# Optimization experiments

Hardware: AMD Instinct MI355X
Metric: run time of the kernel (lower is better)

The kernel has to match this reference:

```python
import jax, jax.numpy as jnp
import numpy as np

NUM_HEADS = 16
LN_EPS = 1e-12


def setup_inputs() -> dict:
    key = jax.random.key(0)
    ks = jax.random.split(key, 4)
    L, B, D = 2048, 2, 1024
    x = jax.random.normal(ks[0], (L, B, D), dtype=jnp.float32)
    attention_mask = jax.random.randint(ks[1], (B, L), 0, 2, dtype=jnp.int32)
    ln_w = jnp.ones((D,), dtype=jnp.float32)
    ln_b = jnp.zeros((D,), dtype=jnp.float32)
    qkv_w = jax.random.normal(ks[2], (3 * D, D), dtype=jnp.float32) * 0.02
    qkv_b = jnp.zeros((3 * D,), dtype=jnp.float32)
    out_w = jax.random.normal(ks[3], (D, D), dtype=jnp.float32) * 0.02
    out_b = jnp.zeros((D,), dtype=jnp.float32)
    return {"x": x, "attention_mask": attention_mask, "ln_w": ln_w, "ln_b": ln_b,
            "qkv_w": qkv_w, "qkv_b": qkv_b, "out_w": out_w, "out_b": out_b}


def _layer_norm(x, w, b):
    mu = jnp.mean(x, axis=-1, keepdims=True)
    var = jnp.mean(jnp.square(x - mu), axis=-1, keepdims=True)
    return (x - mu) * jax.lax.rsqrt(var + LN_EPS) * w + b


def reference(x, attention_mask, ln_w, ln_b, qkv_w, qkv_b, out_w, out_b):
    L, B, D = x.shape
    H = NUM_HEADS
    hd = D // H
    scale = 1.0 / np.sqrt(hd).astype(np.float32)

    xn = _layer_norm(x, ln_w, ln_b)                       # (L, B, D)
    qkv = xn @ qkv_w.T + qkv_b                            # (L, B, 3D)
    q, k, v = jnp.split(qkv, 3, axis=-1)
    # (L, B, D) -> (L, B*H, hd) -> (B*H, L, hd)
    q = q.reshape(L, B * H, hd).swapaxes(0, 1)
    k = k.reshape(L, B * H, hd).swapaxes(0, 1)
    v = v.reshape(L, B * H, hd).swapaxes(0, 1)

    scores = jnp.einsum('nld,nmd->nlm', q, k) * scale     # (B*H, L, L)
    mask = jnp.broadcast_to(attention_mask[:, None, :], (B, H, L)).reshape(B * H, 1, L)
    scores = jnp.where(mask == 0, -jnp.inf, scores)
    probs = jax.nn.softmax(scores, axis=-1)               # masked cols -> 0
    # dropout prob = 0.0 -> identity
    context = jnp.einsum('nlm,nmd->nld', probs, v)        # (B*H, L, hd)
    context = context.swapaxes(0, 1).reshape(L, B, D)
    return context @ out_w.T + out_b
```

## Files before the change

kernel.cpp:

```cpp
#include <hip/hip_runtime.h>
#include <hip/hip_bf16.h>
#include <cstdint>

static constexpr int LSEQ = 2048;
static constexpr int BB   = 2;
static constexpr int DM   = 1024;
static constexpr int NHD  = 16;
static constexpr int HD   = 64;
static constexpr int ROWS = LSEQ * BB;
static constexpr int NQKV = 3 * DM;

typedef __attribute__((ext_vector_type(8)))  short v8s;
typedef __attribute__((ext_vector_type(4)))  float v4f;
typedef __attribute__((ext_vector_type(16))) float v16f;
typedef __attribute__((ext_vector_type(4)))  unsigned int v4u;

#if __has_builtin(__builtin_amdgcn_exp2f)
#define EXP2F(x) __builtin_amdgcn_exp2f(x)
#else
#define EXP2F(x) __expf((x) * 0.69314718056f)
#endif

static constexpr float QSCALE = 0.125f * 1.44269504089f;
static constexpr float NEGM   = -10.0f * 1.44269504089f;

__device__ __forceinline__ unsigned short f2bf(float f) {
    unsigned int u = __builtin_bit_cast(unsigned int, f);
    u += 0x7fffu + ((u >> 16) & 1u);
    return (unsigned short)(u >> 16);
}

__device__ __forceinline__ void gload_lds16(const void* g, void* l) {
    auto gp = (const __attribute__((address_space(1))) unsigned int*)(uintptr_t)g;
    auto lp = (__attribute__((address_space(3))) unsigned int*)(uintptr_t)l;
    __builtin_amdgcn_global_load_lds(gp, lp, 16, 0, 0);
}

__global__ __launch_bounds__(256) void cast_w_kernel(const float* __restrict__ qkv_w,
                                                     const float* __restrict__ out_w,
                                                     unsigned short* __restrict__ wq,
                                                     unsigned short* __restrict__ wo) {
    size_t i = ((size_t)blockIdx.x * 256 + threadIdx.x) * 8;
    const float* src; unsigned short* dst; size_t off;
    if (i < (size_t)NQKV * DM) { src = qkv_w; dst = wq; off = i; }
    else                       { src = out_w; dst = wo; off = i - (size_t)NQKV * DM; }
    float4 a = *(const float4*)(src + off);
    float4 b = *(const float4*)(src + off + 4);
    ushort4 o0, o1;
    o0.x = f2bf(a.x); o0.y = f2bf(a.y); o0.z = f2bf(a.z); o0.w = f2bf(a.w);
    o1.x = f2bf(b.x); o1.y = f2bf(b.y); o1.z = f2bf(b.z); o1.w = f2bf(b.w);
    *(ushort4*)(dst + off)     = o0;
    *(ushort4*)(dst + off + 4) = o1;
}

__global__ __launch_bounds__(256) void ln_cast_kernel(const float* __restrict__ x,
                                                      const float* __restrict__ w,
                                                      const float* __restrict__ bia,
                                                      unsigned short* __restrict__ xn) {
    const int row = blockIdx.x;
    const int t = threadIdx.x;
    const float* xr = x + (size_t)row * DM;
    float4 v = ((const float4*)xr)[t];
    float s  = v.x + v.y + v.z + v.w;
    float sq = v.x*v.x + v.y*v.y + v.z*v.z + v.w*v.w;
    #pragma unroll
    for (int off = 32; off > 0; off >>= 1) {
        s  += __shfl_down(s, off);
        sq += __shfl_down(sq, off);
    }
    __shared__ float red[8];
    const int wv = t >> 6;
    if ((t & 63) == 0) { red[wv] = s; red[4 + wv] = sq; }
    __syncthreads();
    if (t == 0) {
        float S = red[0] + red[1] + red[2] + red[3];
        float Q = red[4] + red[5] + red[6] + red[7];
        float mu  = S * (1.0f / DM);
        float var = Q * (1.0f / DM) - mu * mu;
        red[0] = mu;
        red[1] = rsqrtf(var + 1e-12f);
    }
    __syncthreads();
    const float mu = red[0], rs = red[1];
    float4 wv4 = ((const float4*)w)[t];
    float4 bv4 = ((const float4*)bia)[t];
    ushort4 o;
    o.x = f2bf((v.x - mu) * rs * wv4.x + bv4.x);
    o.y = f2bf((v.y - mu) * rs * wv4.y + bv4.y);
    o.z = f2bf((v.z - mu) * rs * wv4.z + bv4.z);
    o.w = f2bf((v.w - mu) * rs * wv4.w + bv4.w);
    ((ushort4*)(xn + (size_t)row * DM))[t] = o;
}

template <int BM, int BN, int EPI>
__global__ __launch_bounds__(BM == 256 ? 512 : 256)
void gemm2_kernel(const unsigned short* __restrict__ A,
                  const unsigned short* __restrict__ Bt,
                  const float* __restrict__ bias,
                  float* __restrict__ outF,
                  unsigned short* __restrict__ qb,
                  unsigned short* __restrict__ kb,
                  unsigned short* __restrict__ vt,
                  int N) {
    constexpr int K  = DM;
    constexpr int NW = (BM == 256) ? 8 : 4;
    constexpr int NWN = NW / 2;
    constexpr int WM = BM / 2;
    constexpr int WN = BN / NWN;
    constexpr int MR = WM / 16;
    constexpr int FC = WN / 16;
    constexpr int NT = K / 64;
    __shared__ unsigned short Al[2][BM * 64];
    __shared__ unsigned short Bl[2][BN * 64];
    const int nbn = N / BN;
    const int bm = blockIdx.x / nbn;
    const int bn = blockIdx.x % nbn;
    const int tid = threadIdx.x;
    const int w = tid >> 6, lane = tid & 63;
    const int l15 = lane & 15, l4 = lane >> 4;
    const int wm = w / NWN, wn = w % NWN;
    const unsigned short* Ab = A  + (size_t)bm * BM * K;
    const unsigned short* Bb = Bt + (size_t)bn * BN * K;
    const int srow8  = lane >> 3;
    const int schunk = ((lane & 7) ^ (srow8 & 7)) * 8;
    const int swz    = l15 & 7;

    v4f acc[MR][FC] = {};

    auto STAGE = [&](int buf, int t) {
        const int k0 = t * 64;
        #pragma unroll
        for (int i = 0; i < BM / 8 / NW; ++i) {
            const int r0 = w * (BM / NW) + i * 8;
            gload_lds16(Ab + (size_t)(r0 + srow8) * K + k0 + schunk, &Al[buf][r0 * 64]);
        }
        #pragma unroll
        for (int i = 0; i < BN / 8 / NW; ++i) {
            const int r0 = w * (BN / NW) + i * 8;
            gload_lds16(Bb + (size_t)(r0 + srow8) * K + k0 + schunk, &Bl[buf][r0 * 64]);
        }
    };
    auto COMPUTE = [&](int buf) {
        #pragma unroll
        for (int ks = 0; ks < 2; ++ks) {
            v8s af[MR]; v8s bf[FC];
            #pragma unroll
            for (int m = 0; m < MR; ++m) {
                const int row = wm * WM + m * 16 + l15;
                af[m] = *(const v8s*)&Al[buf][row * 64 + ((ks * 4 + l4) ^ swz) * 8];
            }
            #pragma unroll
            for (int n = 0; n < FC; ++n) {
                const int row = wn * WN + n * 16 + l15;
                bf[n] = *(const v8s*)&Bl[buf][row * 64 + ((ks * 4 + l4) ^ swz) * 8];
            }
            #pragma unroll
            for (int m = 0; m < MR; ++m)
                #pragma unroll
                for (int n = 0; n < FC; ++n)
                    acc[m][n] = __builtin_amdgcn_mfma_f32_16x16x32_bf16(af[m], bf[n], acc[m][n], 0, 0, 0);
        }
    };

    STAGE(0, 0);
    __syncthreads();
    int cur = 0;
    for (int t = 0; t < NT - 1; ++t) {
        STAGE(cur ^ 1, t + 1);
        COMPUTE(cur);
        __syncthreads();
        cur ^= 1;
    }
    COMPUTE(cur);

    #pragma unroll
    for (int m = 0; m < MR; ++m) {
        #pragma unroll
        for (int n = 0; n < FC; ++n) {
            #pragma unroll
            for (int r = 0; r < 4; ++r) {
                const int row = bm * BM + wm * WM + m * 16 + l4 * 4 + r;
                const int col = bn * BN + wn * WN + n * 16 + l15;
                const float val = acc[m][n][r] + bias[col];
                if (EPI == 0) {
                    outF[(size_t)row * N + col] = val;
                } else {
                    const int lq = row >> 1, b = row & 1;
                    const int which = col >> 10, jr = col & 1023;
                    const int h = jr >> 6, d = jr & 63;
                    const int bh = b * NHD + h;
                    if (which == 0)      qb[((size_t)bh * LSEQ + lq) * HD + d] = f2bf(val * QSCALE);
                    else if (which == 1) kb[((size_t)bh * LSEQ + lq) * HD + d] = f2bf(val);
                    else                 vt[((size_t)bh * HD + d) * LSEQ + lq] = f2bf(val);
                }
            }
        }
    }
}

__global__ __launch_bounds__(256) void attn_kernel(const unsigned short* __restrict__ qbuf,
                                                   const unsigned short* __restrict__ kbuf,
                                                   const unsigned short* __restrict__ vtbuf,
                                                   const int* __restrict__ amask,
                                                   unsigned short* __restrict__ ctx) {
    __shared__ unsigned short Kl[2][64 * 64];
    __shared__ unsigned short Vl[2][64 * 64];
    __shared__ alignas(16) float mb_all[LSEQ];
    __shared__ alignas(16) float inv_l[4 * 32];
    const int id = blockIdx.x;
    const int inner = id >> 3;
    const int bh = (id & 7) * 4 + (inner & 3);
    const int qblk = inner >> 2;
    const int bat = bh >> 4, h = bh & 15;
    const int tid = threadIdx.x;
    const int w = tid >> 6, lane = tid & 63;
    const int l31 = lane & 31, hi = lane >> 5;
    const int q0 = qblk * 128 + w * 32;

    #pragma unroll
    for (int i = 0; i < LSEQ / 256; ++i)
        mb_all[i * 256 + tid] = amask[bat * LSEQ + i * 256 + tid] ? NEGM : -1e30f;

    const unsigned short* Qp = qbuf + ((size_t)bh * LSEQ + q0 + l31) * HD + hi * 8;
    v8s qfr[4];
    #pragma unroll
    for (int s = 0; s < 4; ++s) qfr[s] = *(const v8s*)(Qp + s * 16);

    const unsigned short* Kb = kbuf  + (size_t)bh * LSEQ * HD;
    const unsigned short* Vb = vtbuf + (size_t)bh * HD * LSEQ;

    v16f O0 = {}, O1 = {};
    float lsum = 0.f;

    const int srow = lane >> 3;
    const int schunk = ((lane & 7) ^ srow) * 8;
    const int rsw = l31 & 7;

    auto STAGE = [&](int buf, int kv0) {
        const int r0 = w * 16;
        gload_lds16(Kb + (size_t)(kv0 + r0 + srow) * HD + schunk,       &Kl[buf][r0 * 64]);
        gload_lds16(Kb + (size_t)(kv0 + r0 + 8 + srow) * HD + schunk,   &Kl[buf][(r0 + 8) * 64]);
        gload_lds16(Vb + (size_t)(r0 + srow) * LSEQ + kv0 + schunk,     &Vl[buf][r0 * 64]);
        gload_lds16(Vb + (size_t)(r0 + 8 + srow) * LSEQ + kv0 + schunk, &Vl[buf][(r0 + 8) * 64]);
    };

    STAGE(0, 0);
    __syncthreads();
    int cur = 0;
    for (int t = 0; t < LSEQ / 64; ++t) {
        if (t + 1 < LSEQ / 64) STAGE(cur ^ 1, (t + 1) * 64);
        const int kv0 = t * 64;

        #pragma unroll
        for (int kvh = 0; kvh < 2; ++kvh) {
            v16f sc = {};
            #pragma unroll
            for (int s = 0; s < 4; ++s) {
                const v8s kf = *(const v8s*)&Kl[cur][(kvh * 32 + l31) * 64 + ((2 * s + hi) ^ rsw) * 8];
                sc = __builtin_amdgcn_mfma_f32_32x32x16_bf16(kf, qfr[s], sc, 0, 0, 0);
            }
            float4 mbv[4];
            #pragma unroll
            for (int g = 0; g < 4; ++g)
                mbv[g] = *(const float4*)&mb_all[kv0 + kvh * 32 + g * 8 + hi * 4];
            float pf[16];
            #pragma unroll
            for (int g = 0; g < 4; ++g) {
                #pragma unroll
                for (int bq = 0; bq < 4; ++bq) {
                    const float mbx = (bq == 0) ? mbv[g].x : (bq == 1) ? mbv[g].y
                                     : (bq == 2) ? mbv[g].z : mbv[g].w;
                    const float p = EXP2F(sc[g * 4 + bq] + mbx);
                    pf[g * 4 + bq] = p;
                    lsum += p;
                }
            }
            #pragma unroll
            for (int c = 0; c < 2; ++c) {
                unsigned int W[4];
                #pragma unroll
                for (int k = 0; k < 4; ++k)
                    asm("v_cvt_pk_bf16_f32 %0, %1, %2"
                        : "=v"(W[k]) : "v"(pf[8 * c + 2 * k]), "v"(pf[8 * c + 2 * k + 1]));
                const unsigned int sel0 = hi ? W[0] : W[2];
                const unsigned int sel1 = hi ? W[1] : W[3];
                const unsigned int S0 = (unsigned int)__shfl_xor((int)sel0, 32);
                const unsigned int S1 = (unsigned int)__shfl_xor((int)sel1, 32);
                v4u fw;
                fw.x = hi ? S0 : W[0];
                fw.y = hi ? S1 : W[1];
                fw.z = hi ? W[2] : S0;
                fw.w = hi ? W[3] : S1;
                const v8s pa = __builtin_bit_cast(v8s, fw);
                const int vch = (kvh * 4 + c * 2 + hi);
                const v8s vf0 = *(const v8s*)&Vl[cur][(l31) * 64      + (vch ^ rsw) * 8];
                const v8s vf1 = *(const v8s*)&Vl[cur][(32 + l31) * 64 + (vch ^ rsw) * 8];
                O0 = __builtin_amdgcn_mfma_f32_32x32x16_bf16(pa, vf0, O0, 0, 0, 0);
                O1 = __builtin_amdgcn_mfma_f32_32x32x16_bf16(pa, vf1, O1, 0, 0, 0);
            }
        }
        __syncthreads();
        cur ^= 1;
    }

    lsum += __shfl_xor(lsum, 32);
    if (hi == 0) inv_l[w * 32 + l31] = 1.0f / lsum;
    asm volatile("s_waitcnt lgkmcnt(0)" ::: "memory");
    __builtin_amdgcn_sched_barrier(0);

    #pragma unroll
    for (int g = 0; g < 4; ++g) {
        const float4 iv = *(const float4*)&inv_l[w * 32 + g * 8 + hi * 4];
        #pragma unroll
        for (int bq = 0; bq < 4; ++bq) {
            const float ivx = (bq == 0) ? iv.x : (bq == 1) ? iv.y : (bq == 2) ? iv.z : iv.w;
            const int lq = q0 + g * 8 + hi * 4 + bq;
            unsigned short* crow = ctx + ((size_t)lq * BB + bat) * DM + h * HD;
            crow[l31]      = f2bf(O0[g * 4 + bq] * ivx);
            crow[32 + l31] = f2bf(O1[g * 4 + bq] * ivx);
        }
    }
}

extern "C" void kernel_launch(void* const* d_in, const int* in_sizes, int n_in,
                              void* d_out, int out_size, void* d_ws, size_t ws_size,
                              hipStream_t stream) {
    (void)in_sizes; (void)n_in; (void)out_size; (void)ws_size;
    const float* x     = (const float*)d_in[0];
    const int*   amask = (const int*)d_in[1];
    const float* ln_w  = (const float*)d_in[2];
    const float* ln_b  = (const float*)d_in[3];
    const float* qkv_w = (const float*)d_in[4];
    const float* qkv_b = (const float*)d_in[5];
    const float* out_w = (const float*)d_in[6];
    const float* out_b = (const float*)d_in[7];
    float* out = (float*)d_out;

    unsigned short* ws    = (unsigned short*)d_ws;
    unsigned short* xn    = ws;
    unsigned short* wq    = xn + (size_t)ROWS * DM;
    unsigned short* wo    = wq + (size_t)NQKV * DM;
    unsigned short* qbuf  = wo + (size_t)DM * DM;
    unsigned short* kbuf  = qbuf + (size_t)BB * NHD * LSEQ * HD;
    unsigned short* vtbuf = kbuf + (size_t)BB * NHD * LSEQ * HD;
    unsigned short* ctx   = vtbuf + (size_t)BB * NHD * LSEQ * HD;

    cast_w_kernel<<<2048, 256, 0, stream>>>(qkv_w, out_w, wq, wo);
    ln_cast_kernel<<<ROWS, 256, 0, stream>>>(x, ln_w, ln_b, xn);
    gemm2_kernel<128, 192, 1><<<(ROWS / 128) * (NQKV / 192), 256, 0, stream>>>(
        xn, wq, qkv_b, nullptr, qbuf, kbuf, vtbuf, NQKV);
    attn_kernel<<<512, 256, 0, stream>>>(qbuf, kbuf, vtbuf, amask, ctx);
    gemm2_kernel<128, 64, 0><<<(ROWS / 128) * (DM / 64), 256, 0, stream>>>(
        ctx, wo, out_b, out, nullptr, nullptr, nullptr, DM);
}
```

Measured before the change: 128.9 us.

## Single-buffer GEMM LDS, smaller QKV tile, XCD-aware block swizzle, raise occupancy

The GEMM kernel drops LDS double buffering for a single buffer with a sync before and after compute, and sets launch bounds to 256 threads with 4 blocks per CU. The QKV projection tile shrinks from 128x192 to 128x96, doubling the grid. Block IDs are remapped so consecutive tiles land on the same XCD for L2 reuse. The aim is more resident waves to hide latency, at the cost of losing load/compute overlap within a block.

```diff
diff --git a/kernel.cpp b/kernel.cpp
--- a/kernel.cpp
+++ b/kernel.cpp
@@ -93,7 +93,7 @@
 }
 
 template <int BM, int BN, int EPI>
-__global__ __launch_bounds__(BM == 256 ? 512 : 256)
+__global__ __launch_bounds__(256, 4)
 void gemm2_kernel(const unsigned short* __restrict__ A,
                   const unsigned short* __restrict__ Bt,
                   const float* __restrict__ bias,
@@ -103,22 +103,22 @@
                   unsigned short* __restrict__ vt,
                   int N) {
     constexpr int K  = DM;
-    constexpr int NW = (BM == 256) ? 8 : 4;
-    constexpr int NWN = NW / 2;
     constexpr int WM = BM / 2;
-    constexpr int WN = BN / NWN;
+    constexpr int WN = BN / 2;
     constexpr int MR = WM / 16;
     constexpr int FC = WN / 16;
     constexpr int NT = K / 64;
-    __shared__ unsigned short Al[2][BM * 64];
-    __shared__ unsigned short Bl[2][BN * 64];
+    __shared__ unsigned short Al[BM * 64];
+    __shared__ unsigned short Bl[BN * 64];
     const int nbn = N / BN;
-    const int bm = blockIdx.x / nbn;
-    const int bn = blockIdx.x % nbn;
+    const int cpx = gridDim.x >> 3;
+    const int sid = (blockIdx.x & 7) * cpx + (blockIdx.x >> 3);
+    const int bm = sid / nbn;
+    const int bn = sid % nbn;
     const int tid = threadIdx.x;
     const int w = tid >> 6, lane = tid & 63;
     const int l15 = lane & 15, l4 = lane >> 4;
-    const int wm = w / NWN, wn = w % NWN;
+    const int wm = w >> 1, wn = w & 1;
     const unsigned short* Ab = A  + (size_t)bm * BM * K;
     const unsigned short* Bb = Bt + (size_t)bn * BN * K;
     const int srow8  = lane >> 3;
@@ -127,32 +127,32 @@
 
     v4f acc[MR][FC] = {};
 
-    auto STAGE = [&](int buf, int t) {
+    auto STAGE = [&](int t) {
         const int k0 = t * 64;
         #pragma unroll
-        for (int i = 0; i < BM / 8 / NW; ++i) {
-            const int r0 = w * (BM / NW) + i * 8;
-            gload_lds16(Ab + (size_t)(r0 + srow8) * K + k0 + schunk, &Al[buf][r0 * 64]);
-        }
-        #pragma unroll
-        for (int i = 0; i < BN / 8 / NW; ++i) {
-            const int r0 = w * (BN / NW) + i * 8;
-            gload_lds16(Bb + (size_t)(r0 + srow8) * K + k0 + schunk, &Bl[buf][r0 * 64]);
+        for (int i = 0; i < BM / 8 / 4; ++i) {
+            const int r0 = w * (BM / 4) + i * 8;
+            gload_lds16(Ab + (size_t)(r0 + srow8) * K + k0 + schunk, &Al[r0 * 64]);
+        }
+        #pragma unroll
+        for (int i = 0; i < BN / 8 / 4; ++i) {
+            const int r0 = w * (BN / 4) + i * 8;
+            gload_lds16(Bb + (size_t)(r0 + srow8) * K + k0 + schunk, &Bl[r0 * 64]);
         }
     };
-    auto COMPUTE = [&](int buf) {
+    auto COMPUTE = [&]() {
         #pragma unroll
         for (int ks = 0; ks < 2; ++ks) {
             v8s af[MR]; v8s bf[FC];
             #pragma unroll
             for (int m = 0; m < MR; ++m) {
                 const int row = wm * WM + m * 16 + l15;
-                af[m] = *(const v8s*)&Al[buf][row * 64 + ((ks * 4 + l4) ^ swz) * 8];
+                af[m] = *(const v8s*)&Al[row * 64 + ((ks * 4 + l4) ^ swz) * 8];
             }
             #pragma unroll
             for (int n = 0; n < FC; ++n) {
                 const int row = wn * WN + n * 16 + l15;
-                bf[n] = *(const v8s*)&Bl[buf][row * 64 + ((ks * 4 + l4) ^ swz) * 8];
+                bf[n] = *(const v8s*)&Bl[row * 64 + ((ks * 4 + l4) ^ swz) * 8];
             }
             #pragma unroll
             for (int m = 0; m < MR; ++m)
@@ -162,16 +162,12 @@
         }
     };
 
-    STAGE(0, 0);
-    __syncthreads();
-    int cur = 0;
-    for (int t = 0; t < NT - 1; ++t) {
-        STAGE(cur ^ 1, t + 1);
-        COMPUTE(cur);
+    for (int t = 0; t < NT; ++t) {
+        STAGE(t);
         __syncthreads();
-        cur ^= 1;
-    }
-    COMPUTE(cur);
+        COMPUTE();
+        __syncthreads();
+    }
 
     #pragma unroll
     for (int m = 0; m < MR; ++m) {
@@ -347,7 +343,7 @@
 
     cast_w_kernel<<<2048, 256, 0, stream>>>(qkv_w, out_w, wq, wo);
     ln_cast_kernel<<<ROWS, 256, 0, stream>>>(x, ln_w, ln_b, xn);
-    gemm2_kernel<128, 192, 1><<<(ROWS / 128) * (NQKV / 192), 256, 0, stream>>>(
+    gemm2_kernel<128, 96, 1><<<(ROWS / 128) * (NQKV / 96), 256, 0, stream>>>(
         xn, wq, qkv_b, nullptr, qbuf, kbuf, vtbuf, NQKV);
     attn_kernel<<<512, 256, 0, stream>>>(qbuf, kbuf, vtbuf, amask, ctx);
     gemm2_kernel<128, 64, 0><<<(ROWS / 128) * (DM / 64), 256, 0, stream>>>(
```

New measurement: 133.1 us. 1.03x slower.
